# Performance work log

Hardware: AMD Instinct MI355X
Metric: run time of the kernel (lower is better)

Reference implementation:

```python
import jax, jax.numpy as jnp
import numpy as np

_SUBPIXEL_EPS = 1e-6


def spiral_pattern(sz_y: int, sz_x: int) -> np.ndarray:
    pattern = np.zeros((2 * sz_y + 1, 2 * sz_x + 1), dtype=np.float32)
    radius = sz_y
    n = 0
    for dy in range(radius + 1):
        for direction in range(4):
            dx_start = -dy
            limit = 1 if direction == 0 and dy == 0 else dy
            for dx in range(dx_start, limit):
                if direction == 0:
                    wx_b, wy_b = radius + dx, radius + dy
                elif direction == 1:
                    wx_b, wy_b = radius + dy, radius - dx
                elif direction == 2:
                    wx_b, wy_b = radius - dx, radius - dy
                else:
                    wx_b, wy_b = radius - dy, radius + dx
                n += 1
                pattern[wy_b, wx_b] = n
    return pattern


def argmin_centered_spiral(x, sz):
    # x: [..., num_ch] float32 cost values; spiral tie-break, no cv_offset.
    num_ch = (2 * sz + 1) ** 2
    min_val = jnp.min(x, axis=-1, keepdims=True)
    default_mask = (x == min_val).astype(jnp.float32)
    central_bias = jnp.asarray(spiral_pattern(sz, sz).reshape(num_ch)) * _SUBPIXEL_EPS
    central = default_mask - central_bias
    mask = (central == jnp.max(central, axis=-1, keepdims=True)).astype(jnp.float32)
    ch_range = jnp.arange(num_ch, dtype=jnp.float32)
    final = mask - ch_range * _SUBPIXEL_EPS
    one_hot = (final == jnp.max(final, axis=-1, keepdims=True)).astype(jnp.float32)
    return jnp.sum(one_hot * ch_range, axis=-1).astype(jnp.int32)


def setup_inputs() -> dict:
    key = jax.random.key(0)
    k1, k2 = jax.random.split(key)
    B, H, W, K = 1, 135, 240, 16
    sr = 4
    C = (2 * sr + 1) ** 2 + 1  # 81 block-match candidates + 1 input-MV channel
    windows = jax.random.randint(k1, (B, H, W, C, K), 0, 256).astype(jnp.float32)
    templates = jax.random.randint(k2, (B, H, W, 1, K), 0, 256).astype(jnp.float32)
    return {"windows": windows, "templates": templates, "search_range": sr}


def reference(windows, templates, search_range):
    B, H, W, C, K = windows.shape
    sr = int(search_range)
    # SAD cost volume (inputs are integer-valued; float32 sums are exact here)
    cost = jnp.sum(jnp.abs(windows - templates), axis=-1)  # [B,H,W,C]
    input_mv_idx = (2 * sr + 1) ** 2
    # motion-vector LUT
    rng = jnp.arange(-sr, sr + 1, dtype=jnp.float32)
    jj, ii = jnp.meshgrid(rng, rng, indexing="ij")
    vec_lut = (-1.0 * jnp.stack([jj, ii], axis=-1).reshape(-1, 2)).astype(jnp.float16)
    # spiral-tie-break argmin over block-match candidates
    idx_bm = argmin_centered_spiral(cost[..., :input_mv_idx], sr)[..., None]  # [B,H,W,1]
    min_cost_bm = jnp.take_along_axis(cost, idx_bm, axis=3)  # [B,H,W,1]
    has_input_mv = (C - 1) == input_mv_idx
    if has_input_mv:
        cost_at_input_mv = cost[..., -1:]
        input_mv_mask = cost_at_input_mv < min_cost_bm
        min_idx = jnp.where(input_mv_mask, input_mv_idx, idx_bm)
        min_cost_volume = jnp.minimum(cost_at_input_mv, min_cost_bm)
    else:
        input_mv_mask = jnp.zeros_like(min_cost_bm, dtype=bool)
        min_idx = idx_bm
        min_cost_volume = min_cost_bm
    vector = vec_lut[idx_bm[..., 0]]  # [B,H,W,2]
    min_templates = jnp.take_along_axis(windows, min_idx[..., None], axis=3)  # [B,H,W,1,K]
    return (vector, min_templates, input_mv_mask, min_cost_volume.astype(jnp.int32))
```

## Files before the change

kernel.cpp:

```cpp
#include <hip/hip_runtime.h>

#define KDIM 16
#define NSPIRAL 81

__device__ __constant__ int d_spiral[NSPIRAL] = {
 74,73,72,71,70,69,68,67,66,
 75,44,43,42,41,40,39,38,65,
 76,45,22,21,20,19,18,37,64,
 77,46,23, 8, 7, 6,17,36,63,
 78,47,24, 9, 1, 5,16,35,62,
 79,48,25, 2, 3, 4,15,34,61,
 80,49,10,11,12,13,14,33,60,
 81,26,27,28,29,30,31,32,59,
 50,51,52,53,54,55,56,57,58
};

__global__ __launch_bounds__(256) void calc_vector_kernel(
    const float* __restrict__ windows,
    const float* __restrict__ templates,
    float* __restrict__ out,
    int npix, int C)
{
    __shared__ int s_spiral[NSPIRAL];
    const int tid = threadIdx.x;
    if (tid < NSPIRAL) s_spiral[tid] = d_spiral[tid];
    __syncthreads();

    const int wave = tid >> 6;
    const int lane = tid & 63;
    const int pix = blockIdx.x * 4 + wave;
    if (pix >= npix) return;

    const int rowlen = C * KDIM;
    const int nf4 = rowlen >> 2;
    const float* wrow = windows + (size_t)pix * rowlen;

    const int kseg = (lane & 3) * 4;
    const float4 t4 = *reinterpret_cast<const float4*>(templates + (size_t)pix * KDIM + kseg);

    int bestkey = 0x7FFFFFFF;
    int cost81 = 0;

    #pragma unroll
    for (int it = 0; it < 6; ++it) {
        const int f = it * 64 + lane;
        const int c = it * 16 + (lane >> 2);
        float s = 0.0f;
        if (f < nf4) {
            const float4 w4 = *reinterpret_cast<const float4*>(wrow + f * 4);
            s = fabsf(w4.x - t4.x) + fabsf(w4.y - t4.y) +
                fabsf(w4.z - t4.z) + fabsf(w4.w - t4.w);
        }
        s += __shfl_xor(s, 1);
        s += __shfl_xor(s, 2);
        const int cost = (int)s;
        if (f < nf4 && c < NSPIRAL) {
            const int n = s_spiral[c];
            const int key = (cost << 14) | (n << 7) | c;
            bestkey = min(bestkey, key);
        }
        if (c == NSPIRAL && f < nf4) cost81 = cost;
    }

    #pragma unroll
    for (int off = 32; off >= 1; off >>= 1)
        bestkey = min(bestkey, __shfl_xor(bestkey, off));
    cost81 = __shfl(cost81, 4);

    const int idx_bm      = bestkey & 127;
    const int min_cost_bm = bestkey >> 14;
    const bool mv_mask    = cost81 < min_cost_bm;
    const int min_idx     = mv_mask ? NSPIRAL : idx_bm;
    const int mcv         = min(cost81, min_cost_bm);

    float* out_vec  = out;
    float* out_tmpl = out + (size_t)npix * 2;
    float* out_mask = out + (size_t)npix * 18;
    float* out_cost = out + (size_t)npix * 19;

    if (lane < 4) {
        const float4 w4 = *reinterpret_cast<const float4*>(wrow + min_idx * KDIM + lane * 4);
        *reinterpret_cast<float4*>(out_tmpl + (size_t)pix * KDIM + lane * 4) = w4;
    }
    if (lane == 0) {
        out_vec[(size_t)pix * 2 + 0] = (float)(4 - idx_bm / 9);
        out_vec[(size_t)pix * 2 + 1] = (float)(4 - idx_bm % 9);
        out_mask[pix] = mv_mask ? 1.0f : 0.0f;
        out_cost[pix] = (float)mcv;
    }
}

extern "C" void kernel_launch(void* const* d_in, const int* in_sizes, int n_in,
                              void* d_out, int out_size, void* d_ws, size_t ws_size,
                              hipStream_t stream) {
    const float* windows   = (const float*)d_in[0];
    const float* templates = (const float*)d_in[1];
    float* out = (float*)d_out;

    const int npix = in_sizes[1] / KDIM;
    const int C    = in_sizes[0] / in_sizes[1];

    const int blocks = (npix + 3) / 4;
    calc_vector_kernel<<<blocks, 256, 0, stream>>>(windows, templates, out, npix, C);
}
```

Measured before the change: 33.18 us.

## Add persistent double-buffered C=82 kernel with nontemporal loads and stores

Adds a specialised kernel for C=82 that launches a capped grid of persistent waves, each looping over pixels and prefetching the next pixel's window row into registers while the current one is reduced. Global loads and output stores use nontemporal hints, spiral keys are precomputed per lane, and the shared-memory spiral table with its block barrier is removed. The intent is to keep more memory requests in flight for this bandwidth-bound streaming kernel. The cost is higher register pressure from two buffered pixels and less parallelism from the fixed grid size.

```diff
diff --git a/kernel.cpp b/kernel.cpp
--- a/kernel.cpp
+++ b/kernel.cpp
@@ -2,6 +2,9 @@
 
 #define KDIM 16
 #define NSPIRAL 81
+
+typedef float f4 __attribute__((ext_vector_type(4)));
+typedef float f2 __attribute__((ext_vector_type(2)));
 
 __device__ __constant__ int d_spiral[NSPIRAL] = {
  74,73,72,71,70,69,68,67,66,
@@ -15,17 +18,118 @@
  50,51,52,53,54,55,56,57,58
 };
 
-__global__ __launch_bounds__(256) void calc_vector_kernel(
+__device__ __forceinline__ f4 ntload4(const float* p) {
+    return __builtin_nontemporal_load(reinterpret_cast<const f4*>(p));
+}
+
+struct Pix { f4 a[6]; f4 t; };
+
+
+__device__ __forceinline__ void load_pix82(const float* __restrict__ windows,
+                                           const float* __restrict__ templates,
+                                           int pix, int lane, Pix& P)
+{
+    const float* wrow = windows + (size_t)pix * 1312;
+    P.t = ntload4(templates + (size_t)pix * KDIM + (lane & 3) * 4);
+    #pragma unroll
+    for (int it = 0; it < 5; ++it)
+        P.a[it] = ntload4(wrow + (it * 64 + lane) * 4);
+    P.a[5] = f4{0.f, 0.f, 0.f, 0.f};
+    if (lane < 8) P.a[5] = ntload4(wrow + (320 + lane) * 4);
+}
+
+__device__ __forceinline__ void process_pix82(const Pix& P, const int* nb, int lane,
+    int pix, int npix, const float* __restrict__ windows, float* __restrict__ out)
+{
+    int bk = 0x7FFFFFFF;
+    int c81 = 0;
+    #pragma unroll
+    for (int it = 0; it < 6; ++it) {
+        float s = fabsf(P.a[it].x - P.t.x) + fabsf(P.a[it].y - P.t.y)
+                + fabsf(P.a[it].z - P.t.z) + fabsf(P.a[it].w - P.t.w);
+        s += __shfl_xor(s, 1);
+        s += __shfl_xor(s, 2);
+        const int cost = (int)s;
+        if (it < 5) {
+            bk = min(bk, (cost << 14) | nb[it]);
+        } else {
+            if (lane < 4)        bk = min(bk, (cost << 14) | nb[5]);
+            if ((lane >> 2) == 1) c81 = cost;
+        }
+    }
+    #pragma unroll
+    for (int off = 32; off >= 1; off >>= 1)
+        bk = min(bk, __shfl_xor(bk, off));
+    c81 = __shfl(c81, 4);
+
+    const int idx = bk & 127, mc = bk >> 14;
+    const bool m  = c81 < mc;
+    const int mi  = m ? NSPIRAL : idx;
+    const int mcv = min(c81, mc);
+
+    float* out_vec  = out;
+    float* out_tmpl = out + (size_t)npix * 2;
+    float* out_mask = out + (size_t)npix * 18;
+    float* out_cost = out + (size_t)npix * 19;
+
+    if (lane < 4) {
+        const f4 w = *reinterpret_cast<const f4*>(
+            windows + (size_t)pix * 1312 + mi * KDIM + lane * 4);
+        __builtin_nontemporal_store(w,
+            reinterpret_cast<f4*>(out_tmpl + (size_t)pix * KDIM + lane * 4));
+    }
+    if (lane == 0) {
+        f2 v; v.x = (float)(4 - idx / 9); v.y = (float)(4 - idx % 9);
+        __builtin_nontemporal_store(v, reinterpret_cast<f2*>(out_vec + (size_t)pix * 2));
+        __builtin_nontemporal_store(m ? 1.0f : 0.0f, out_mask + pix);
+        __builtin_nontemporal_store((float)mcv, out_cost + pix);
+    }
+}
+
+__global__ __launch_bounds__(256, 4) void calc_vector82(
+    const float* __restrict__ windows,
+    const float* __restrict__ templates,
+    float* __restrict__ out, int npix)
+{
+    const int lane = threadIdx.x & 63;
+    const int gw = (int)((blockIdx.x * blockDim.x + threadIdx.x) >> 6);
+    const int nw = (int)((gridDim.x * blockDim.x) >> 6);
+
+    int nb[6];
+    #pragma unroll
+    for (int it = 0; it < 6; ++it) {
+        const int c = it * 16 + (lane >> 2);
+        nb[it] = (c < NSPIRAL) ? ((d_spiral[c] << 7) | c) : 0;
+    }
+
+    int pix = gw;
+    if (pix >= npix) return;
+    Pix A, B;
+    load_pix82(windows, templates, pix, lane, A);
+
+    while (true) {
+        int nxt = pix + nw;
+        if (nxt < npix) load_pix82(windows, templates, nxt, lane, B);
+        process_pix82(A, nb, lane, pix, npix, windows, out);
+        pix = nxt;
+        if (pix >= npix) return;
+
+        nxt = pix + nw;
+        if (nxt < npix) load_pix82(windows, templates, nxt, lane, A);
+        process_pix82(B, nb, lane, pix, npix, windows, out);
+        pix = nxt;
+        if (pix >= npix) return;
+    }
+}
+
+
+__global__ __launch_bounds__(256) void calc_vector_generic(
     const float* __restrict__ windows,
     const float* __restrict__ templates,
     float* __restrict__ out,
     int npix, int C)
 {
-    __shared__ int s_spiral[NSPIRAL];
     const int tid = threadIdx.x;
-    if (tid < NSPIRAL) s_spiral[tid] = d_spiral[tid];
-    __syncthreads();
-
     const int wave = tid >> 6;
     const int lane = tid & 63;
     const int pix = blockIdx.x * 4 + wave;
@@ -36,7 +140,7 @@
     const float* wrow = windows + (size_t)pix * rowlen;
 
     const int kseg = (lane & 3) * 4;
-    const float4 t4 = *reinterpret_cast<const float4*>(templates + (size_t)pix * KDIM + kseg);
+    const f4 t4 = ntload4(templates + (size_t)pix * KDIM + kseg);
 
     int bestkey = 0x7FFFFFFF;
     int cost81 = 0;
@@ -46,20 +150,20 @@
         const int f = it * 64 + lane;
         const int c = it * 16 + (lane >> 2);
         float s = 0.0f;
-        if (f < nf4) {
-            const float4 w4 = *reinterpret_cast<const float4*>(wrow + f * 4);
+        const bool act = f < nf4;
+        if (act) {
+            const f4 w4 = ntload4(wrow + f * 4);
             s = fabsf(w4.x - t4.x) + fabsf(w4.y - t4.y) +
                 fabsf(w4.z - t4.z) + fabsf(w4.w - t4.w);
         }
         s += __shfl_xor(s, 1);
         s += __shfl_xor(s, 2);
         const int cost = (int)s;
-        if (f < nf4 && c < NSPIRAL) {
-            const int n = s_spiral[c];
-            const int key = (cost << 14) | (n << 7) | c;
+        if (act && c < NSPIRAL) {
+            const int key = (cost << 14) | (d_spiral[c] << 7) | c;
             bestkey = min(bestkey, key);
         }
-        if (c == NSPIRAL && f < nf4) cost81 = cost;
+        if (act && c == NSPIRAL) cost81 = cost;
     }
 
     #pragma unroll
@@ -67,11 +171,11 @@
         bestkey = min(bestkey, __shfl_xor(bestkey, off));
     cost81 = __shfl(cost81, 4);
 
-    const int idx_bm      = bestkey & 127;
-    const int min_cost_bm = bestkey >> 14;
-    const bool mv_mask    = cost81 < min_cost_bm;
-    const int min_idx     = mv_mask ? NSPIRAL : idx_bm;
-    const int mcv         = min(cost81, min_cost_bm);
+    const int idx = bestkey & 127, mc = bestkey >> 14;
+    const bool hasmv = (C == NSPIRAL + 1);
+    const bool m  = hasmv && (cost81 < mc);
+    const int mi  = m ? NSPIRAL : idx;
+    const int mcv = m ? cost81 : mc;
 
     float* out_vec  = out;
     float* out_tmpl = out + (size_t)npix * 2;
@@ -79,14 +183,15 @@
     float* out_cost = out + (size_t)npix * 19;
 
     if (lane < 4) {
-        const float4 w4 = *reinterpret_cast<const float4*>(wrow + min_idx * KDIM + lane * 4);
-        *reinterpret_cast<float4*>(out_tmpl + (size_t)pix * KDIM + lane * 4) = w4;
+        const f4 w = *reinterpret_cast<const f4*>(wrow + mi * KDIM + lane * 4);
+        __builtin_nontemporal_store(w,
+            reinterpret_cast<f4*>(out_tmpl + (size_t)pix * KDIM + lane * 4));
     }
     if (lane == 0) {
-        out_vec[(size_t)pix * 2 + 0] = (float)(4 - idx_bm / 9);
-        out_vec[(size_t)pix * 2 + 1] = (float)(4 - idx_bm % 9);
-        out_mask[pix] = mv_mask ? 1.0f : 0.0f;
-        out_cost[pix] = (float)mcv;
+        f2 v; v.x = (float)(4 - idx / 9); v.y = (float)(4 - idx % 9);
+        __builtin_nontemporal_store(v, reinterpret_cast<f2*>(out_vec + (size_t)pix * 2));
+        __builtin_nontemporal_store(m ? 1.0f : 0.0f, out_mask + pix);
+        __builtin_nontemporal_store((float)mcv, out_cost + pix);
     }
 }
 
@@ -100,6 +205,12 @@
     const int npix = in_sizes[1] / KDIM;
     const int C    = in_sizes[0] / in_sizes[1];
 
-    const int blocks = (npix + 3) / 4;
-    calc_vector_kernel<<<blocks, 256, 0, stream>>>(windows, templates, out, npix, C);
-}
+    if (C == 82) {
+        int blocks = (npix + 3) / 4;
+        if (blocks > 1024) blocks = 1024;
+        calc_vector82<<<blocks, 256, 0, stream>>>(windows, templates, out, npix);
+    } else {
+        const int blocks = (npix + 3) / 4;
+        calc_vector_generic<<<blocks, 256, 0, stream>>>(windows, templates, out, npix, C);
+    }
+}
```

Result: slower. 35.42 us (+6.8%).
